# Kernel tuning notes

Measured on AMD Instinct MI355X. Metric: run time of the kernel, lower is better.

## Reference

```python
import jax, jax.numpy as jnp
import numpy as np

B, S, D = 2, 2048, 2048
H = 16
HD = D // H            # 128 head dim
L = 512                # latent dim
R = 64                 # rope dim (min(64, HD) = 64)
RH = R // 2
SCALE = HD ** -0.5     # note: uses head_dim, not head_dim+rope_dim
NEG = jnp.float32(-1e9)


def _rope_tables():
    inv_freq = 1.0 / (10000.0 ** (jnp.arange(0, R, 2, dtype=jnp.float32) / R))  # [RH]
    pos = jnp.arange(S, dtype=jnp.float32)
    freqs = pos[:, None] * inv_freq[None, :]  # [S, RH]
    return jnp.cos(freqs), jnp.sin(freqs)


def _apply_rope(x, cos, sin):
    # x: [B, H, S, R], interleaved even/odd rotation as in the torch source
    xe, xo = x[..., 0::2], x[..., 1::2]                    # [B,H,S,RH]
    c = cos[None, None]
    s = sin[None, None]
    re = xe * c - xo * s
    ro = xe * s + xo * c
    return jnp.stack([re, ro], axis=-1).reshape(x.shape)   # re-interleave


def setup_inputs() -> dict:
    key = jax.random.key(0)
    ks = jax.random.split(key, 8)
    std = 0.02
    f32 = jnp.float32
    return {
        "x":     jax.random.normal(ks[0], (B, S, D), f32),
        "W_ckv": jax.random.normal(ks[1], (D, L), f32) * std,      # compress_kv
        "W_kv":  jax.random.normal(ks[2], (L, 2 * D), f32) * std,  # kv_proj
        "W_cq":  jax.random.normal(ks[3], (D, L), f32) * std,      # compress_q
        "W_q":   jax.random.normal(ks[4], (L, D), f32) * std,      # q_proj
        "W_qr":  jax.random.normal(ks[5], (L, H * R), f32) * std,  # q_rope
        "W_kr":  jax.random.normal(ks[6], (L, R), f32) * std,      # k_rope
        "W_out": jax.random.normal(ks[7], (D, D), f32) * std,      # out_proj
    }


def reference(x, W_ckv, W_kv, W_cq, W_q, W_qr, W_kr, W_out):
    cos, sin = _rope_tables()

    c_kv = x @ W_ckv                                   # [B,S,L]
    kv = c_kv @ W_kv                                   # [B,S,2D]
    c_q = x @ W_cq                                     # [B,S,L]

    q_c = (c_q @ W_q).reshape(B, S, H, HD).transpose(0, 2, 1, 3)    # [B,H,S,HD]
    q_r = (c_q @ W_qr).reshape(B, S, H, R).transpose(0, 2, 1, 3)    # [B,H,S,R]
    k_r = (c_kv @ W_kr)[:, None, :, :]                               # [B,1,S,R]

    k_c, v = jnp.split(kv, 2, axis=-1)
    k_c = k_c.reshape(B, S, H, HD).transpose(0, 2, 1, 3)             # [B,H,S,HD]
    v = v.reshape(B, S, H, HD).transpose(0, 2, 1, 3)                 # [B,H,S,HD]

    q_r = _apply_rope(q_r, cos, sin)
    k_r = jnp.broadcast_to(_apply_rope(k_r, cos, sin), (B, H, S, R))

    q = jnp.concatenate([q_c, q_r], axis=-1)                         # [B,H,S,HD+R]
    k = jnp.concatenate([k_c, k_r], axis=-1)                         # [B,H,S,HD+R]

    scores = jnp.einsum("bhqd,bhkd->bhqk", q, k) * SCALE             # [B,H,S,S]
    causal = jnp.tril(jnp.ones((S, S), dtype=bool))
    scores = jnp.where(causal[None, None], scores, NEG)
    p = jax.nn.softmax(scores, axis=-1)
    attended = jnp.einsum("bhqk,bhkd->bhqd", p, v)                   # [B,H,S,HD]

    out = attended.transpose(0, 2, 1, 3).reshape(B, S, D) @ W_out    # [B,S,D]
    return out  # dropout is identity in eval / p=0
```

## Files before the change

kernel.cpp:

```cpp
#include <hip/hip_runtime.h>
#include <hip/hip_bf16.h>
#include <cstdint>
#include <cstddef>

typedef __bf16 bf16;
typedef __attribute__((ext_vector_type(2))) __bf16 bf16x2;
typedef __attribute__((ext_vector_type(4))) __bf16 bf16x4;
typedef __attribute__((ext_vector_type(8))) __bf16 bf16x8;
typedef __attribute__((ext_vector_type(4))) float f32x4;

#define MFMA16(a, b, c) __builtin_amdgcn_mfma_f32_16x16x32_bf16((a), (b), (c), 0, 0, 0)
#define SCALE_L2E 0.127517432f

#define QCR_STRIDE 3072
#define KV_STRIDE  4160

__device__ __forceinline__ void gload16(const void* g, void* l) {
    __builtin_amdgcn_global_load_lds(
        (const __attribute__((address_space(1))) void*)g,
        (__attribute__((address_space(3))) void*)l, 16, 0, 0);
}

__device__ __forceinline__ void bar_lgkm() {
    asm volatile("s_waitcnt lgkmcnt(0)" ::: "memory");
    __builtin_amdgcn_s_barrier();
    asm volatile("" ::: "memory");
}

__global__ void k_cvt(const float* __restrict__ in, bf16* __restrict__ out, int n4)
{
    int i = blockIdx.x * blockDim.x + threadIdx.x;
    int stride = gridDim.x * blockDim.x;
    const float4* in4 = (const float4*)in;
    bf16x4* o4 = (bf16x4*)out;
    for (; i < n4; i += stride) {
        float4 v = in4[i];
        bf16x4 o;
        o[0] = (bf16)v.x; o[1] = (bf16)v.y; o[2] = (bf16)v.z; o[3] = (bf16)v.w;
        o4[i] = o;
    }
}

__global__ __launch_bounds__(256) void k_cvtT(const float* __restrict__ in,
                                              bf16* __restrict__ out, int Kd, int Nd)
{
    __shared__ float tile[32][33];
    const int k0 = blockIdx.y * 32, n0 = blockIdx.x * 32;
    const int t = threadIdx.x;
    const int r = t >> 3, c4 = (t & 7) * 4;
    float4 v = *(const float4*)(in + (size_t)(k0 + r) * Nd + n0 + c4);
    tile[r][c4 + 0] = v.x; tile[r][c4 + 1] = v.y;
    tile[r][c4 + 2] = v.z; tile[r][c4 + 3] = v.w;
    __syncthreads();
    bf16x4 o;
    o[0] = (bf16)tile[c4 + 0][r]; o[1] = (bf16)tile[c4 + 1][r];
    o[2] = (bf16)tile[c4 + 2][r]; o[3] = (bf16)tile[c4 + 3][r];
    *(bf16x4*)(out + (size_t)(n0 + r) * Kd + k0 + c4) = o;
}

template<int NF, bool F32OUT>
__global__ __launch_bounds__(256) void k_gemm_bt(
    const bf16* __restrict__ A, const bf16* __restrict__ BT,
    bf16* __restrict__ Cb, float* __restrict__ Cf,
    int M, int N, int K, int lda, float cscale)
{
    __shared__ bf16 As[2][4096];
    __shared__ bf16 Bs[2][NF * 1024];

    const int t = threadIdx.x;
    const int m0 = blockIdx.y * 128;
    const int n0 = blockIdx.x * (NF * 32);
    const int wid = t >> 6, lane = t & 63;
    const int wm = (wid >> 1) * 64, wn = (wid & 1) * (NF * 16);
    const int lr = lane & 15, lk = (lane >> 4) * 8;

    const int srow = t >> 2, skc = (t & 3) << 3;
    const int bn0 = min(n0 + srow, N - 1);
    const int bn1 = min(n0 + srow + 64, N - 1);

    f32x4 acc[4][NF];
    const f32x4 z = {0.f, 0.f, 0.f, 0.f};
#pragma unroll
    for (int m = 0; m < 4; ++m)
#pragma unroll
        for (int n = 0; n < NF; ++n) acc[m][n] = z;

    auto stage = [&](int buf, int k0) {
        gload16(BT + (size_t)bn0 * K + k0 + skc, &Bs[buf][t * 8]);
        if constexpr (NF == 4)
            gload16(BT + (size_t)bn1 * K + k0 + skc, &Bs[buf][(t + 256) * 8]);
        gload16(A + (size_t)(m0 + srow) * lda + k0 + skc, &As[buf][t * 8]);
        gload16(A + (size_t)(m0 + srow + 64) * lda + k0 + skc, &As[buf][(t + 256) * 8]);
    };

    stage(0, 0);
    __syncthreads();

    for (int k0 = 0; k0 < K; k0 += 32) {
        const int cur = (k0 >> 5) & 1;
        if (k0 + 32 < K) stage(cur ^ 1, k0 + 32);

        bf16x8 af[4], bfr[NF];
#pragma unroll
        for (int m = 0; m < 4; ++m) af[m] = *(const bf16x8*)(&As[cur][(wm + m * 16 + lr) * 32 + lk]);
#pragma unroll
        for (int n = 0; n < NF; ++n) bfr[n] = *(const bf16x8*)(&Bs[cur][(wn + n * 16 + lr) * 32 + lk]);
#pragma unroll
        for (int m = 0; m < 4; ++m)
#pragma unroll
            for (int n = 0; n < NF; ++n)
                acc[m][n] = MFMA16(af[m], bfr[n], acc[m][n]);

        __syncthreads();
    }

    const int lrow4 = (lane >> 4) * 4;
#pragma unroll
    for (int m = 0; m < 4; ++m)
#pragma unroll
        for (int n = 0; n < NF; ++n)
#pragma unroll
            for (int i = 0; i < 4; ++i) {
                int r = m0 + wm + m * 16 + lrow4 + i;
                int c = n0 + wn + n * 16 + lr;
                if (r < M && c < N) {
                    float val = acc[m][n][i] * cscale;
                    if constexpr (F32OUT) Cf[(size_t)r * N + c] = val;
                    else Cb[(size_t)r * N + c] = (bf16)val;
                }
            }
}

__global__ void k_rope_q(bf16* __restrict__ qcr)
{
    int idx = blockIdx.x * blockDim.x + threadIdx.x;
    int row = idx >> 9;
    int rem = idx & 511;
    int h = rem >> 5;
    int i = rem & 31;
    int s = row & 2047;
    float ang = (float)s * __expf(-(float)i * 0.28782313662f);
    float c = cosf(ang), sn = sinf(ang);
    size_t base = (size_t)row * QCR_STRIDE + 2048 + h * 64 + (i << 1);
    float xe = (float)qcr[base], xo = (float)qcr[base + 1];
    qcr[base] = (bf16)(xe * c - xo * sn);
    qcr[base + 1] = (bf16)(xe * sn + xo * c);
}

__global__ void k_rope_k(bf16* __restrict__ kvkr)
{
    int idx = blockIdx.x * blockDim.x + threadIdx.x;
    int row = idx >> 5;
    int i = idx & 31;
    int s = row & 2047;
    float ang = (float)s * __expf(-(float)i * 0.28782313662f);
    float c = cosf(ang), sn = sinf(ang);
    size_t base = (size_t)row * KV_STRIDE + 4096 + (i << 1);
    float xe = (float)kvkr[base], xo = (float)kvkr[base + 1];
    kvkr[base] = (bf16)(xe * c - xo * sn);
    kvkr[base + 1] = (bf16)(xe * sn + xo * c);
}

__global__ __launch_bounds__(512, 4) void k_attn(
    const bf16* __restrict__ qcr, const bf16* __restrict__ kvkr,
    bf16* __restrict__ att)
{
    __shared__ bf16 Ks[64 * 200];
    __shared__ bf16 Vt[128 * 72];
    __shared__ bf16 Pw[8][16 * 72];

    const int L = blockIdx.x;
    const int base = L & 255;
    const int bh = base & 31;
    const int qtg = base >> 5;
    const int qt = (L < 256) ? qtg : 15 - qtg;
    const int h = bh & 15, b = bh >> 4;

    const int t = threadIdx.x;
    const int wid = t >> 6, lane = t & 63;
    const int lr = lane & 15, lk = (lane >> 4) * 8, lrow4 = (lane >> 4) * 4;
    const size_t rowbase = (size_t)b * 2048;

    const int kcrow = t >> 4, kcfc = (t & 15) << 3;
    const int krrow = t >> 3, krfc = (t & 7) << 3;
    const int vk = (t & 31) * 2;
    const int vf = (t >> 5) * 8;

    const f32x4 z = {0.f, 0.f, 0.f, 0.f};

    bf16x8 rc0, rc1, rr, rv0, rv1;
    auto LOAD = [&](int kb) {
        rc0 = *(const bf16x8*)(kvkr + (rowbase + kb + kcrow) * KV_STRIDE + h * 128 + kcfc);
        rc1 = *(const bf16x8*)(kvkr + (rowbase + kb + kcrow + 32) * KV_STRIDE + h * 128 + kcfc);
        rr  = *(const bf16x8*)(kvkr + (rowbase + kb + krrow) * KV_STRIDE + 4096 + krfc);
        const bf16* vs = kvkr + (rowbase + kb + vk) * KV_STRIDE + 2048 + h * 128 + vf;
        rv0 = *(const bf16x8*)vs;
        rv1 = *(const bf16x8*)(vs + KV_STRIDE);
    };
    auto WRITE = [&]() {
        *(bf16x8*)(Ks + kcrow * 200 + kcfc) = rc0;
        *(bf16x8*)(Ks + (kcrow + 32) * 200 + kcfc) = rc1;
        *(bf16x8*)(Ks + krrow * 200 + 128 + krfc) = rr;
#pragma unroll
        for (int j = 0; j < 8; ++j) {
            bf16x2 pr; pr[0] = rv0[j]; pr[1] = rv1[j];
            *(bf16x2*)(Vt + (vf + j) * 72 + vk) = pr;
        }
    };

    const int qrow_w = qt * 128 + wid * 16;

    bf16x8 qf[6];
    {
        const size_t qrow = rowbase + qrow_w + lr;
        const bf16* qp = qcr + qrow * QCR_STRIDE + h * 128;
#pragma unroll
        for (int ks = 0; ks < 4; ++ks) qf[ks] = *(const bf16x8*)(qp + ks * 32 + lk);
        const bf16* qp2 = qcr + qrow * QCR_STRIDE + 2048 + h * 64;
#pragma unroll
        for (int ks = 0; ks < 2; ++ks) qf[4 + ks] = *(const bf16x8*)(qp2 + ks * 32 + lk);
    }

    bf16x8 ones;
#pragma unroll
    for (int j = 0; j < 8; ++j) ones[j] = (bf16)1.0f;

    float mrow[4], lsum[4];
    f32x4 o[8];
#pragma unroll
    for (int i = 0; i < 4; ++i) { mrow[i] = -3e38f; lsum[i] = 0.f; }
#pragma unroll
    for (int n = 0; n < 8; ++n) o[n] = z;

    const int nkt = 2 * qt + 2;
    LOAD(0);

#pragma unroll 1
    for (int kt = 0; kt < nkt; ++kt) {
        const int kb = kt * 64;
        bar_lgkm();
        WRITE();
        if (kt + 1 < nkt) LOAD(kb + 64);
        bar_lgkm();

        if (kb > qrow_w + 15) continue;

        f32x4 sacc[4];
#pragma unroll
        for (int kg = 0; kg < 4; ++kg) {
            f32x4 s = z;
#pragma unroll
            for (int ks = 0; ks < 6; ++ks) {
                bf16x8 kf = *(const bf16x8*)(Ks + (kg * 16 + lr) * 200 + ks * 32 + lk);
                s = MFMA16(qf[ks], kf, s);
            }
            sacc[kg] = s;
        }

        const bool domask = (kb + 63) > qrow_w;
        float rmax[4];
#pragma unroll
        for (int i = 0; i < 4; ++i) {
            int qi = qrow_w + lrow4 + i;
            float mx = -3e38f;
#pragma unroll
            for (int kg = 0; kg < 4; ++kg) {
                float v = sacc[kg][i];
                if (domask && (kb + kg * 16 + lr) > qi) v = -3e38f;
                sacc[kg][i] = v;
                mx = fmaxf(mx, v);
            }
            rmax[i] = mx;
        }
#pragma unroll
        for (int d = 1; d < 16; d <<= 1)
#pragma unroll
            for (int i = 0; i < 4; ++i)
                rmax[i] = fmaxf(rmax[i], __shfl_xor(rmax[i], d, 64));

        int anynew = 0;
#pragma unroll
        for (int i = 0; i < 4; ++i)
            if (rmax[i] > mrow[i]) anynew = 1;
        if (__any(anynew)) {
#pragma unroll
            for (int i = 0; i < 4; ++i) {
                float mnew = fmaxf(mrow[i], rmax[i]);
                float scl = __builtin_amdgcn_exp2f(mrow[i] - mnew);
                mrow[i] = mnew;
                lsum[i] *= scl;
#pragma unroll
                for (int n = 0; n < 8; ++n) o[n][i] *= scl;
            }
        }

#pragma unroll
        for (int kg = 0; kg < 4; ++kg)
#pragma unroll
            for (int i = 0; i < 4; ++i)
                sacc[kg][i] = __builtin_amdgcn_exp2f(sacc[kg][i] - mrow[i]);

#pragma unroll
        for (int kg = 0; kg < 4; ++kg)
#pragma unroll
            for (int i = 0; i < 4; ++i)
                Pw[wid][(lrow4 + i) * 72 + kg * 16 + lr] = (bf16)sacc[kg][i];

        f32x4 rs = z;
#pragma unroll
        for (int ks = 0; ks < 2; ++ks) {
            bf16x8 pa = *(const bf16x8*)(&Pw[wid][lr * 72 + ks * 32 + lk]);
            rs = MFMA16(pa, ones, rs);
#pragma unroll
            for (int n = 0; n < 8; ++n) {
                bf16x8 vfr = *(const bf16x8*)(Vt + (n * 16 + lr) * 72 + ks * 32 + lk);
                o[n] = MFMA16(pa, vfr, o[n]);
            }
        }
#pragma unroll
        for (int i = 0; i < 4; ++i) lsum[i] += rs[i];
    }

#pragma unroll
    for (int i = 0; i < 4; ++i) {
        float inv = 1.f / lsum[i];
        size_t orow = (rowbase + qrow_w + lrow4 + i) * 2048 + h * 128;
#pragma unroll
        for (int n = 0; n < 8; ++n)
            att[orow + n * 16 + lr] = (bf16)(o[n][i] * inv);
    }
}

extern "C" void kernel_launch(void* const* d_in, const int* in_sizes, int n_in,
                              void* d_out, int out_size, void* d_ws, size_t ws_size,
                              hipStream_t stream)
{
    (void)in_sizes; (void)n_in; (void)out_size; (void)ws_size;
    const float* x = (const float*)d_in[0];
    const float* w_ckv = (const float*)d_in[1];
    const float* w_kv = (const float*)d_in[2];
    const float* w_cq = (const float*)d_in[3];
    const float* w_q = (const float*)d_in[4];
    const float* w_qr = (const float*)d_in[5];
    const float* w_kr = (const float*)d_in[6];
    const float* w_out = (const float*)d_in[7];
    float* out = (float*)d_out;

    char* ws = (char*)d_ws;
    size_t off = 0;
    auto take = [&](size_t elems) -> bf16* {
        bf16* p = (bf16*)(ws + off);
        off += (elems * sizeof(bf16) + 255) & ~(size_t)255;
        return p;
    };
    bf16* WCT    = take(1024ull * 2048);
    bf16* WKVKRT = take(4160ull * 512);
    bf16* WQQRT  = take(3072ull * 512);
    bf16* C      = take(4096ull * 1024);
    bf16* KVKR   = take(4096ull * 4160);
    bf16* QCR    = take(4096ull * 3072);
    bf16* ATT    = take(4096ull * 2048);
    bf16* WOUTT  = C;
    bf16* XB     = KVKR;

    auto cvtT = [&](const float* in, bf16* o, int K, int N) {
        k_cvtT<<<dim3(N / 32, K / 32), 256, 0, stream>>>(in, o, K, N);
    };
    cvtT(w_ckv, WCT, 2048, 512);
    cvtT(w_cq, WCT + 512ull * 2048, 2048, 512);
    cvtT(w_kv, WKVKRT, 512, 4096);
    cvtT(w_kr, WKVKRT + 4096ull * 512, 512, 64);
    cvtT(w_q, WQQRT, 512, 2048);
    cvtT(w_qr, WQQRT + 2048ull * 512, 512, 1024);

    k_cvt<<<2048, 256, 0, stream>>>(x, XB, (4096 * 2048) / 4);

    k_gemm_bt<2, false><<<dim3(16, 32), 256, 0, stream>>>(
        XB, WCT, C, nullptr, 4096, 1024, 2048, 2048, 1.0f);
    k_gemm_bt<4, false><<<dim3(33, 32), 256, 0, stream>>>(
        C, WKVKRT, KVKR, nullptr, 4096, 4160, 512, 1024, 1.0f);
    k_gemm_bt<4, false><<<dim3(24, 32), 256, 0, stream>>>(
        C + 512, WQQRT, QCR, nullptr, 4096, 3072, 512, 1024, SCALE_L2E);

    cvtT(w_out, WOUTT, 2048, 2048);

    k_rope_q<<<8192, 256, 0, stream>>>(QCR);
    k_rope_k<<<512, 256, 0, stream>>>(KVKR);

    k_attn<<<512, 512, 0, stream>>>(QCR, KVKR, ATT);

    k_gemm_bt<4, true><<<dim3(16, 32), 256, 0, stream>>>(
        ATT, WOUTT, nullptr, out, 4096, 2048, 2048, 2048, 1.0f);
}
```

Before: 304.3 us.

## Shrink attention query tile to 64 rows, swizzle K in LDS, reorder blocks

The attention kernel now uses 256-thread blocks that each cover a 64-row query tile, launching 1024 blocks scheduled longest-first instead of 512 blocks of 128 rows with paired scheduling. The K tile is split into separate content and rope LDS buffers with an XOR swizzle instead of padded rows, which is meant to avoid LDS bank conflicts while using less shared memory. Smaller tiles give finer load balance for the causal workload and better occupancy, but each K/V tile is now reused by fewer query rows, so global loads per query rise.

Result: faster. 294.7 us (-3.2%).

```diff
diff --git a/kernel.cpp b/kernel.cpp
--- a/kernel.cpp
+++ b/kernel.cpp
@@ -161,54 +161,77 @@
     kvkr[base + 1] = (bf16)(xe * sn + xo * c);
 }
 
-__global__ __launch_bounds__(512, 4) void k_attn(
+__global__ __launch_bounds__(256, 4) void k_attn(
     const bf16* __restrict__ qcr, const bf16* __restrict__ kvkr,
     bf16* __restrict__ att)
 {
-    __shared__ bf16 Ks[64 * 200];
+    __shared__ bf16 Ksc[64 * 128];
+    __shared__ bf16 Ksr[64 * 64];
     __shared__ bf16 Vt[128 * 72];
-    __shared__ bf16 Pw[8][16 * 72];
+    __shared__ bf16 Pw[4][16 * 72];
 
     const int L = blockIdx.x;
-    const int base = L & 255;
-    const int bh = base & 31;
-    const int qtg = base >> 5;
-    const int qt = (L < 256) ? qtg : 15 - qtg;
+    const int qt = 31 - (L >> 5);
+    const int bh = L & 31;
     const int h = bh & 15, b = bh >> 4;
 
     const int t = threadIdx.x;
     const int wid = t >> 6, lane = t & 63;
     const int lr = lane & 15, lk = (lane >> 4) * 8, lrow4 = (lane >> 4) * 4;
+    const int lq = lane >> 4;
     const size_t rowbase = (size_t)b * 2048;
 
-    const int kcrow = t >> 4, kcfc = (t & 15) << 3;
-    const int krrow = t >> 3, krfc = (t & 7) << 3;
+    const f32x4 z = {0.f, 0.f, 0.f, 0.f};
+
     const int vk = (t & 31) * 2;
     const int vf = (t >> 5) * 8;
 
-    const f32x4 z = {0.f, 0.f, 0.f, 0.f};
-
-    bf16x8 rc0, rc1, rr, rv0, rv1;
+    bf16x8 rc[4], rr[2], rv[4];
     auto LOAD = [&](int kb) {
-        rc0 = *(const bf16x8*)(kvkr + (rowbase + kb + kcrow) * KV_STRIDE + h * 128 + kcfc);
-        rc1 = *(const bf16x8*)(kvkr + (rowbase + kb + kcrow + 32) * KV_STRIDE + h * 128 + kcfc);
-        rr  = *(const bf16x8*)(kvkr + (rowbase + kb + krrow) * KV_STRIDE + 4096 + krfc);
-        const bf16* vs = kvkr + (rowbase + kb + vk) * KV_STRIDE + 2048 + h * 128 + vf;
-        rv0 = *(const bf16x8*)vs;
-        rv1 = *(const bf16x8*)(vs + KV_STRIDE);
+#pragma unroll
+        for (int i = 0; i < 4; ++i) {
+            int bb = t + 256 * i;
+            int row = bb >> 4, gcb = bb & 15;
+            rc[i] = *(const bf16x8*)(kvkr + (rowbase + kb + row) * KV_STRIDE + h * 128 + gcb * 8);
+        }
+#pragma unroll
+        for (int i = 0; i < 2; ++i) {
+            int bb = t + 256 * i;
+            int row = bb >> 3, gcb = bb & 7;
+            rr[i] = *(const bf16x8*)(kvkr + (rowbase + kb + row) * KV_STRIDE + 4096 + gcb * 8);
+        }
+#pragma unroll
+        for (int i = 0; i < 2; ++i) {
+            const bf16* vs = kvkr + (rowbase + kb + vk) * KV_STRIDE + 2048 + h * 128 + vf + 64 * i;
+            rv[2 * i]     = *(const bf16x8*)vs;
+            rv[2 * i + 1] = *(const bf16x8*)(vs + KV_STRIDE);
+        }
     };
     auto WRITE = [&]() {
-        *(bf16x8*)(Ks + kcrow * 200 + kcfc) = rc0;
-        *(bf16x8*)(Ks + (kcrow + 32) * 200 + kcfc) = rc1;
-        *(bf16x8*)(Ks + krrow * 200 + 128 + krfc) = rr;
-#pragma unroll
-        for (int j = 0; j < 8; ++j) {
-            bf16x2 pr; pr[0] = rv0[j]; pr[1] = rv1[j];
-            *(bf16x2*)(Vt + (vf + j) * 72 + vk) = pr;
-        }
+#pragma unroll
+        for (int i = 0; i < 4; ++i) {
+            int bb = t + 256 * i;
+            int row = bb >> 4, gcb = bb & 15;
+            int scb = (gcb & 8) | ((gcb ^ row) & 7);
+            *(bf16x8*)(Ksc + row * 128 + scb * 8) = rc[i];
+        }
+#pragma unroll
+        for (int i = 0; i < 2; ++i) {
+            int bb = t + 256 * i;
+            int row = bb >> 3, gcb = bb & 7;
+            int scb = (gcb ^ row) & 7;
+            *(bf16x8*)(Ksr + row * 64 + scb * 8) = rr[i];
+        }
+#pragma unroll
+        for (int i = 0; i < 2; ++i)
+#pragma unroll
+            for (int j = 0; j < 8; ++j) {
+                bf16x2 pr; pr[0] = rv[2 * i][j]; pr[1] = rv[2 * i + 1][j];
+                *(bf16x2*)(Vt + (vf + 64 * i + j) * 72 + vk) = pr;
+            }
     };
 
-    const int qrow_w = qt * 128 + wid * 16;
+    const int qrow_w = qt * 64 + wid * 16;
 
     bf16x8 qf[6];
     {
@@ -232,7 +255,7 @@
 #pragma unroll
     for (int n = 0; n < 8; ++n) o[n] = z;
 
-    const int nkt = 2 * qt + 2;
+    const int nkt = qt + 1;
     LOAD(0);
 
 #pragma unroll 1
@@ -249,10 +272,20 @@
 #pragma unroll
         for (int kg = 0; kg < 4; ++kg) {
             f32x4 s = z;
-#pragma unroll
-            for (int ks = 0; ks < 6; ++ks) {
-                bf16x8 kf = *(const bf16x8*)(Ks + (kg * 16 + lr) * 200 + ks * 32 + lk);
+            const int key = kg * 16 + lr;
+#pragma unroll
+            for (int ks = 0; ks < 4; ++ks) {
+                int cb = ks * 4 + lq;
+                int scb = (cb & 8) | ((cb ^ key) & 7);
+                bf16x8 kf = *(const bf16x8*)(Ksc + key * 128 + scb * 8);
                 s = MFMA16(qf[ks], kf, s);
+            }
+#pragma unroll
+            for (int ks = 0; ks < 2; ++ks) {
+                int cb = ks * 4 + lq;
+                int scb = (cb ^ key) & 7;
+                bf16x8 kf = *(const bf16x8*)(Ksr + key * 64 + scb * 8);
+                s = MFMA16(qf[4 + ks], kf, s);
             }
             sacc[kg] = s;
         }
@@ -387,7 +420,7 @@
     k_rope_q<<<8192, 256, 0, stream>>>(QCR);
     k_rope_k<<<512, 256, 0, stream>>>(KVKR);
 
-    k_attn<<<512, 512, 0, stream>>>(QCR, KVKR, ATT);
+    k_attn<<<1024, 256, 0, stream>>>(QCR, KVKR, ATT);
 
     k_gemm_bt<4, true><<<dim3(16, 32), 256, 0, stream>>>(
         ATT, WOUTT, nullptr, out, 4096, 2048, 2048, 2048, 1.0f);
```
